# Kernel tuning notes

Hardware: AMD Instinct MI355X
Metric: run time of the kernel (lower is better)

The kernel has to match this reference:

```python
import jax, jax.numpy as jnp
import numpy as np

B = 32768
S = 1024          # max_seq_len
DF = 0.99         # discount_factor
AL = 0.95         # advantage_lambda


def _grad_scale(x, s):
    # forward: identity; backward: grad * s (mirrors GradScaler.apply)
    return s * x + jax.lax.stop_gradient((1.0 - s) * x)


def setup_inputs() -> dict:
    key = jax.random.key(0)
    k1, k2 = jax.random.split(key, 2)
    values = jax.random.normal(k1, (B, S + 1, 1), dtype=jnp.float32)
    rewards = jax.random.normal(k2, (B, S, 1), dtype=jnp.float32)
    dones = jnp.zeros((B, S, 1), dtype=jnp.float32)
    raw_gamma = jnp.zeros((1,), dtype=jnp.float32)
    raw_lambd = jnp.zeros((S,), dtype=jnp.float32)
    return {"values": values, "rewards": rewards, "dones": dones,
            "raw_gamma": raw_gamma, "raw_lambd": raw_lambd}


def reference(values, rewards, dones, raw_gamma, raw_lambd):
    # dynamic gamma (scalar) and per-timestep lambda, as in the properties
    gamma = _grad_scale(DF + (1.0 - DF) * (2.0 * jax.nn.sigmoid(raw_gamma) - 1.0), 1.0)[0]
    lam = _grad_scale(AL + (1.0 - AL) * (2.0 * jax.nn.sigmoid(raw_lambd) - 1.0), 0.5)  # [S]

    # time-major views for the scan: [S, B, 1]
    r_tm = jnp.swapaxes(rewards, 0, 1)
    d_tm = jnp.swapaxes(dones, 0, 1)
    v_next_tm = jnp.swapaxes(values[:, 1:], 0, 1)  # values[:, t+1]

    init = (jnp.zeros_like(values[:, -1]), values[:, -1])  # (sum_rewards[S], lambda_returns[S]=values[:, -1])

    def step(carry, xs):
        sr_next, lr_next = carry
        r_t, d_t, v_t, lam_t = xs
        g = gamma * (1.0 - d_t)
        # sum_rewards computed under no_grad in the original
        sr = jax.lax.stop_gradient(r_t + g * (lam_t * sr_next))
        lr = r_t + g * ((1.0 - lam_t) * v_t + lam_t * lr_next)
        return (sr, lr), (sr, lr)

    # backward recurrence over time; outputs returned in forward time order
    _, (sum_r_tm, lam_ret_tm) = jax.lax.scan(step, init, (r_tm, d_tm, v_next_tm, lam), reverse=True)

    lambda_returns = jnp.swapaxes(lam_ret_tm, 0, 1)  # [B, S, 1] == original [:, :-1]
    sum_rewards = jnp.swapaxes(sum_r_tm, 0, 1)       # [B, S, 1]
    return lambda_returns, sum_rewards
```

## Files before the change

kernel.cpp:

```cpp
#include <hip/hip_runtime.h>
#include <math.h>


#define DF_C 0.99f
#define AL_C 0.95f

__global__ __launch_bounds__(256) void td_scan_kernel(
    const float* __restrict__ values,
    const float* __restrict__ rewards,
    const float* __restrict__ dones,
    const float* __restrict__ raw_gamma,
    const float* __restrict__ raw_lambd,
    float* __restrict__ out,
    int B, int S)
{
    const int b   = blockIdx.x;
    const int tid = threadIdx.x;
    const int t0  = tid * 4;

    const float rg    = raw_gamma[0];
    const float sg    = 1.0f / (1.0f + expf(-rg));
    const float gamma = DF_C + (1.0f - DF_C) * (2.0f * sg - 1.0f);

    const size_t rbase = (size_t)b * S + t0;
    const float4 r4 = *reinterpret_cast<const float4*>(rewards + rbase);
    const float4 d4 = *reinterpret_cast<const float4*>(dones   + rbase);
    float r[4] = {r4.x, r4.y, r4.z, r4.w};
    float d[4] = {d4.x, d4.y, d4.z, d4.w};

    const float* vrow = values + (size_t)b * (S + 1);
    float v[4], lam[4];
#pragma unroll
    for (int j = 0; j < 4; ++j) {
        v[j] = vrow[t0 + j + 1];
        const float x = raw_lambd[t0 + j];
        const float s = 1.0f / (1.0f + expf(-x));
        lam[j] = AL_C + (1.0f - AL_C) * (2.0f * s - 1.0f);
    }

    float Al = 0.0f, As = 0.0f, Bp = 1.0f;
#pragma unroll
    for (int j = 0; j < 4; ++j) {
        const float g  = gamma * (1.0f - d[j]);
        const float bt = g * lam[j];
        const float at = r[j] + g * (1.0f - lam[j]) * v[j];
        Al = Al + Bp * at;
        As = As + Bp * r[j];
        Bp = Bp * bt;
    }

    __shared__ float sAl[256], sAs[256], sB[256];
    sAl[tid] = Al; sAs[tid] = As; sB[tid] = Bp;
    __syncthreads();
#pragma unroll
    for (int off = 1; off < 256; off <<= 1) {
        float al = 0.0f, as_ = 0.0f, bb = 1.0f;
        const bool valid = (tid + off) < 256;
        if (valid) { al = sAl[tid + off]; as_ = sAs[tid + off]; bb = sB[tid + off]; }
        __syncthreads();
        if (valid) {
            const float mb = sB[tid];
            sAl[tid] = sAl[tid] + mb * al;
            sAs[tid] = sAs[tid] + mb * as_;
            sB[tid]  = mb * bb;
        }
        __syncthreads();
    }

    float Aex_l = 0.0f, Aex_s = 0.0f, Bex = 1.0f;
    if (tid < 255) { Aex_l = sAl[tid + 1]; Aex_s = sAs[tid + 1]; Bex = sB[tid + 1]; }

    const float v_last = vrow[S];
    float lr = Aex_l + Bex * v_last;
    float sr = Aex_s;

    float out_lr[4], out_sr[4];
#pragma unroll
    for (int j = 3; j >= 0; --j) {
        const float g  = gamma * (1.0f - d[j]);
        const float bt = g * lam[j];
        sr = r[j] + bt * sr;
        lr = r[j] + g * (1.0f - lam[j]) * v[j] + bt * lr;
        out_lr[j] = lr;
        out_sr[j] = sr;
    }

    *reinterpret_cast<float4*>(out + rbase) =
        make_float4(out_lr[0], out_lr[1], out_lr[2], out_lr[3]);
    *reinterpret_cast<float4*>(out + (size_t)B * S + rbase) =
        make_float4(out_sr[0], out_sr[1], out_sr[2], out_sr[3]);
}

extern "C" void kernel_launch(void* const* d_in, const int* in_sizes, int n_in,
                              void* d_out, int out_size, void* d_ws, size_t ws_size,
                              hipStream_t stream) {
    const float* values    = (const float*)d_in[0];
    const float* rewards   = (const float*)d_in[1];
    const float* dones     = (const float*)d_in[2];
    const float* raw_gamma = (const float*)d_in[3];
    const float* raw_lambd = (const float*)d_in[4];
    float* out = (float*)d_out;

    const int S = in_sizes[4];
    const int B = in_sizes[1] / S;

    dim3 grid(B);
    dim3 block(S / 4);
    td_scan_kernel<<<grid, block, 0, stream>>>(values, rewards, dones,
                                               raw_gamma, raw_lambd, out, B, S);
}
```

Measured before the change: 509.8 us.

## Replace shared-memory block scan with wavefront shuffle scan and precompute lambda

```diff
diff --git a/kernel.cpp b/kernel.cpp
--- a/kernel.cpp
+++ b/kernel.cpp
@@ -5,90 +5,110 @@
 #define DF_C 0.99f
 #define AL_C 0.95f
 
+__global__ void td_precompute_kernel(const float* __restrict__ raw_gamma,
+                                     const float* __restrict__ raw_lambd,
+                                     float* __restrict__ ws, int S) {
+    const int t = blockIdx.x * blockDim.x + threadIdx.x;
+    if (t < S) {
+        const float s = 1.0f / (1.0f + expf(-raw_lambd[t]));
+        ws[t] = AL_C + (1.0f - AL_C) * (2.0f * s - 1.0f);
+    }
+    if (t == 0) {
+        const float s = 1.0f / (1.0f + expf(-raw_gamma[0]));
+        ws[S] = DF_C + (1.0f - DF_C) * (2.0f * s - 1.0f);
+    }
+}
+
 __global__ __launch_bounds__(256) void td_scan_kernel(
     const float* __restrict__ values,
     const float* __restrict__ rewards,
     const float* __restrict__ dones,
-    const float* __restrict__ raw_gamma,
-    const float* __restrict__ raw_lambd,
+    const float* __restrict__ lam_g,
     float* __restrict__ out,
     int B, int S)
 {
-    const int b   = blockIdx.x;
-    const int tid = threadIdx.x;
-    const int t0  = tid * 4;
+    const int b    = blockIdx.x;
+    const int tid  = threadIdx.x;
+    const int lane = tid & 63;
+    const int w    = tid >> 6;
+    const int t0   = tid * 4;
 
-    const float rg    = raw_gamma[0];
-    const float sg    = 1.0f / (1.0f + expf(-rg));
-    const float gamma = DF_C + (1.0f - DF_C) * (2.0f * sg - 1.0f);
+    const float gamma = lam_g[S];
 
     const size_t rbase = (size_t)b * S + t0;
     const float4 r4 = *reinterpret_cast<const float4*>(rewards + rbase);
     const float4 d4 = *reinterpret_cast<const float4*>(dones   + rbase);
-    float r[4] = {r4.x, r4.y, r4.z, r4.w};
-    float d[4] = {d4.x, d4.y, d4.z, d4.w};
+    const float4 l4 = *reinterpret_cast<const float4*>(lam_g   + t0);
+    const float* vrow = values + (size_t)b * (S + 1);
 
-    const float* vrow = values + (size_t)b * (S + 1);
-    float v[4], lam[4];
-#pragma unroll
-    for (int j = 0; j < 4; ++j) {
-        v[j] = vrow[t0 + j + 1];
-        const float x = raw_lambd[t0 + j];
-        const float s = 1.0f / (1.0f + expf(-x));
-        lam[j] = AL_C + (1.0f - AL_C) * (2.0f * s - 1.0f);
-    }
+    float r[4]  = {r4.x, r4.y, r4.z, r4.w};
+    float dd[4] = {d4.x, d4.y, d4.z, d4.w};
+    float lm[4] = {l4.x, l4.y, l4.z, l4.w};
+    float bt[4], c[4];
 
     float Al = 0.0f, As = 0.0f, Bp = 1.0f;
 #pragma unroll
     for (int j = 0; j < 4; ++j) {
-        const float g  = gamma * (1.0f - d[j]);
-        const float bt = g * lam[j];
-        const float at = r[j] + g * (1.0f - lam[j]) * v[j];
-        Al = Al + Bp * at;
-        As = As + Bp * r[j];
-        Bp = Bp * bt;
+        const float vv = vrow[t0 + j + 1];
+        const float g  = gamma * (1.0f - dd[j]);
+        bt[j] = g * lm[j];
+        c[j]  = g * (1.0f - lm[j]) * vv;
+        Al += Bp * (r[j] + c[j]);
+        As += Bp * r[j];
+        Bp *= bt[j];
     }
 
-    __shared__ float sAl[256], sAs[256], sB[256];
-    sAl[tid] = Al; sAs[tid] = As; sB[tid] = Bp;
-    __syncthreads();
+    float al = Al, as_ = As, bb = Bp;
 #pragma unroll
-    for (int off = 1; off < 256; off <<= 1) {
-        float al = 0.0f, as_ = 0.0f, bb = 1.0f;
-        const bool valid = (tid + off) < 256;
-        if (valid) { al = sAl[tid + off]; as_ = sAs[tid + off]; bb = sB[tid + off]; }
-        __syncthreads();
-        if (valid) {
-            const float mb = sB[tid];
-            sAl[tid] = sAl[tid] + mb * al;
-            sAs[tid] = sAs[tid] + mb * as_;
-            sB[tid]  = mb * bb;
-        }
-        __syncthreads();
+    for (int off = 1; off < 64; off <<= 1) {
+        float pal = __shfl_down(al,  off, 64);
+        float pas = __shfl_down(as_, off, 64);
+        float pbb = __shfl_down(bb,  off, 64);
+        const bool valid = (lane + off) < 64;
+        pal = valid ? pal : 0.0f;
+        pas = valid ? pas : 0.0f;
+        pbb = valid ? pbb : 1.0f;
+        al  = al  + bb * pal;
+        as_ = as_ + bb * pas;
+        bb  = bb  * pbb;
     }
 
-    float Aex_l = 0.0f, Aex_s = 0.0f, Bex = 1.0f;
-    if (tid < 255) { Aex_l = sAl[tid + 1]; Aex_s = sAs[tid + 1]; Bex = sB[tid + 1]; }
+    __shared__ float wAl[4], wAs[4], wB[4];
+    if (lane == 0) { wAl[w] = al; wAs[w] = as_; wB[w] = bb; }
+
+    float eal = __shfl_down(al,  1, 64);
+    float eas = __shfl_down(as_, 1, 64);
+    float ebb = __shfl_down(bb,  1, 64);
+    if (lane == 63) { eal = 0.0f; eas = 0.0f; ebb = 1.0f; }
+
+    __syncthreads();
+
+    float EAl = 0.0f, EAs = 0.0f, EB = 1.0f;
+    for (int u = w + 1; u < 4; ++u) {
+        EAl = EAl + EB * wAl[u];
+        EAs = EAs + EB * wAs[u];
+        EB  = EB * wB[u];
+    }
 
     const float v_last = vrow[S];
-    float lr = Aex_l + Bex * v_last;
-    float sr = Aex_s;
+    const float lr0 = EAl + EB * v_last;
+    const float sr0 = EAs;
 
-    float out_lr[4], out_sr[4];
+    float lr = eal + ebb * lr0;
+    float sr = eas + ebb * sr0;
+
+    float olr[4], osr[4];
 #pragma unroll
     for (int j = 3; j >= 0; --j) {
-        const float g  = gamma * (1.0f - d[j]);
-        const float bt = g * lam[j];
-        sr = r[j] + bt * sr;
-        lr = r[j] + g * (1.0f - lam[j]) * v[j] + bt * lr;
-        out_lr[j] = lr;
-        out_sr[j] = sr;
+        sr = r[j] + bt[j] * sr;
+        lr = r[j] + c[j] + bt[j] * lr;
+        olr[j] = lr;
+        osr[j] = sr;
     }
-
     *reinterpret_cast<float4*>(out + rbase) =
-        make_float4(out_lr[0], out_lr[1], out_lr[2], out_lr[3]);
+        make_float4(olr[0], olr[1], olr[2], olr[3]);
     *reinterpret_cast<float4*>(out + (size_t)B * S + rbase) =
-        make_float4(out_sr[0], out_sr[1], out_sr[2], out_sr[3]);
+        make_float4(osr[0], osr[1], osr[2], osr[3]);
 }
 
 extern "C" void kernel_launch(void* const* d_in, const int* in_sizes, int n_in,
@@ -100,12 +120,11 @@
     const float* raw_gamma = (const float*)d_in[3];
     const float* raw_lambd = (const float*)d_in[4];
     float* out = (float*)d_out;
+    float* ws  = (float*)d_ws;
 
     const int S = in_sizes[4];
     const int B = in_sizes[1] / S;
 
-    dim3 grid(B);
-    dim3 block(S / 4);
-    td_scan_kernel<<<grid, block, 0, stream>>>(values, rewards, dones,
-                                               raw_gamma, raw_lambd, out, B, S);
+    td_precompute_kernel<<<(S + 255) / 256, 256, 0, stream>>>(raw_gamma, raw_lambd, ws, S);
+    td_scan_kernel<<<B, S / 4, 0, stream>>>(values, rewards, dones, ws, out, B, S);
 }
```

Result: no change. 511.4 us (+0.3%).
